# Optimization experiments

Measured on AMD Instinct MI355X. Metric: run time of the kernel, lower is better.

Reference implementation:

```python
import jax, jax.numpy as jnp
import numpy as np

B, S, D = 4, 2048, 1024  # batch, seq_len, input_dimension
KD, VD = 1024, 1024      # key_dim, value_dim


def setup_inputs() -> dict:
    key = jax.random.key(0)
    ks = jax.random.split(key, 9)
    sc_in = 1.0 / np.sqrt(D)
    sc_v = 1.0 / np.sqrt(VD)
    return {
        "x":  jax.random.normal(ks[0], (B, S, D), dtype=jnp.float32),
        "Wq": jax.random.normal(ks[1], (KD, D), dtype=jnp.float32) * sc_in,
        "bq": jax.random.normal(ks[2], (KD,), dtype=jnp.float32) * 0.01,
        "Wk": jax.random.normal(ks[3], (KD, D), dtype=jnp.float32) * sc_in,
        "bk": jax.random.normal(ks[4], (KD,), dtype=jnp.float32) * 0.01,
        "Wv": jax.random.normal(ks[5], (VD, D), dtype=jnp.float32) * sc_in,
        "bv": jax.random.normal(ks[6], (VD,), dtype=jnp.float32) * 0.01,
        "Wo": jax.random.normal(ks[7], (D, VD), dtype=jnp.float32) * sc_v,
        "bo": jax.random.normal(ks[8], (D,), dtype=jnp.float32) * 0.01,
    }


def reference(x, Wq, bq, Wk, bk, Wv, bv, Wo, bo):
    # projections (torch Linear: x @ W.T + b)
    q = jnp.einsum('bsd,kd->bsk', x, Wq) + bq   # (B,S,KD)
    k = jnp.einsum('bsd,kd->bsk', x, Wk) + bk   # (B,S,KD)
    v = jnp.einsum('bsd,vd->bsv', x, Wv) + bv   # (B,S,VD)

    scores = jnp.einsum('bqk,bsk->bqs', q, k) / jnp.sqrt(jnp.float32(KD))  # (B,S,S)

    # sign rescale: scores * sign(scores) (sign(0) mapped to 1) == |scores| with zeros kept
    sign_mask = jnp.sign(scores)
    sign_mask = sign_mask + (sign_mask == 0).astype(jnp.float32)

    # causal mask: lower-triangular (incl diag) multiplied by 1, strict upper -> -inf
    seq = scores.shape[-1]
    causal = jnp.tril(jnp.ones((seq, seq), dtype=bool))
    masked = jnp.where(causal, scores * sign_mask, -jnp.inf)

    weights = jax.nn.softmax(masked, axis=2)            # (B,S,S)
    out = jnp.einsum('bqs,bsv->bqv', weights, v)        # (B,S,VD)
    return jnp.einsum('bqv,dv->bqd', out, Wo) + bo      # (B,S,D)
```

## Files before the change

kernel.cpp:

```cpp
#include <hip/hip_runtime.h>
#include <hip/hip_bf16.h>
#include <cstdint>


#define BM 128

typedef __attribute__((ext_vector_type(8))) __bf16 bf16x8;
typedef __attribute__((ext_vector_type(4))) __bf16 bf16x4;
typedef __attribute__((ext_vector_type(4))) float floatx4;

struct Ptr3 { const float* p[3]; };

__device__ __forceinline__ void async_copy16(const __bf16* g, const __bf16* l) {
  __builtin_amdgcn_global_load_lds(
      (const __attribute__((address_space(1))) unsigned int*)(const void*)g,
      (__attribute__((address_space(3))) unsigned int*)(unsigned)(uintptr_t)(const void*)l,
      16, 0, 0);
}

__device__ __forceinline__ void gemm_core(const __bf16* __restrict__ pA,
                                          const __bf16* __restrict__ pB,
                                          int K, int kBeg, int kEnd, int mb,
                                          int nb, floatx4 (&acc)[4][4]) {
  __shared__ __align__(16) __bf16 As[3][BM * 32];
  __shared__ __align__(16) __bf16 Bs[3][BM * 32];

  const int t = threadIdx.x;
  const int lane = t & 63;
  const int wave = t >> 6;
  const int quad = lane >> 4;
  const int l16 = lane & 15;
  const int wm = wave >> 1;
  const int wn = wave & 1;
  const int qsw = quad ^ ((l16 >> 1) & 3);

  const int srow = t >> 2;
  const int scol = ((t & 3) ^ ((t >> 3) & 3)) * 8;
  const __bf16* gA = pA + (long)(mb * BM + srow) * K + scol;
  const __bf16* gB = pB + (long)(nb * BM + srow) * K + scol;
  const long rowHalf = (long)64 * K;

  auto stage = [&](int kk, int buf) {
    const long ko = (long)kk * 32;
    __bf16* lA = &As[buf][t * 8];
    __bf16* lB = &Bs[buf][t * 8];
    async_copy16(gA + ko, lA);
    async_copy16(gA + ko + rowHalf, lA + 2048);
    async_copy16(gB + ko, lB);
    async_copy16(gB + ko + rowHalf, lB + 2048);
  };

  stage(kBeg, 0);
  stage(kBeg + 1 < kEnd ? kBeg + 1 : kEnd - 1, 1);

  for (int kk = kBeg; kk < kEnd; ++kk) {
    const int cur = (kk - kBeg) % 3;
    asm volatile("s_waitcnt vmcnt(4)" ::: "memory");
    __builtin_amdgcn_s_barrier();
    __builtin_amdgcn_sched_barrier(0);
    {
      const int nxt = kk + 2;
      stage(nxt < kEnd ? nxt : kEnd - 1, (cur + 2) % 3);
    }
    const __bf16* Asp = &As[cur][0];
    const __bf16* Bsp = &Bs[cur][0];
    bf16x8 af[4], bfr[4];
#pragma unroll
    for (int i = 0; i < 4; ++i) {
      af[i] = *(const bf16x8*)&Asp[(wm * 64 + i * 16 + l16) * 32 + qsw * 8];
      bfr[i] = *(const bf16x8*)&Bsp[(wn * 64 + i * 16 + l16) * 32 + qsw * 8];
    }
#pragma unroll
    for (int i = 0; i < 4; ++i)
#pragma unroll
      for (int j = 0; j < 4; ++j)
        acc[i][j] = __builtin_amdgcn_mfma_f32_16x16x32_bf16(af[i], bfr[j],
                                                            acc[i][j], 0, 0, 0);
  }
  __syncthreads();
}

__device__ __forceinline__ void gemm_core256(const __bf16* __restrict__ pA,
                                             const __bf16* __restrict__ pB,
                                             int K, int kBeg, int kEnd, int mb,
                                             int nb, floatx4 (&acc)[8][4]) {
  __shared__ __align__(16) __bf16 As[3][256 * 32];
  __shared__ __align__(16) __bf16 Bs[3][256 * 32];

  const int t = threadIdx.x;
  const int lane = t & 63;
  const int wave = t >> 6;
  const int quad = lane >> 4;
  const int l16 = lane & 15;
  const int wm = wave >> 2;
  const int wn = wave & 3;
  const int qsw = quad ^ ((l16 >> 1) & 3);

  const int srow = t >> 2;
  const int scol = ((t & 3) ^ ((t >> 3) & 3)) * 8;
  const __bf16* gA = pA + (long)(mb * 256 + srow) * K + scol;
  const __bf16* gB = pB + (long)(nb * 256 + srow) * K + scol;
  const long rowHalf = (long)128 * K;

  auto stage = [&](int kk, int buf) {
    const long ko = (long)kk * 32;
    __bf16* lA = &As[buf][t * 8];
    __bf16* lB = &Bs[buf][t * 8];
    async_copy16(gA + ko, lA);
    async_copy16(gA + ko + rowHalf, lA + 4096);
    async_copy16(gB + ko, lB);
    async_copy16(gB + ko + rowHalf, lB + 4096);
  };

  stage(kBeg, 0);
  stage(kBeg + 1 < kEnd ? kBeg + 1 : kEnd - 1, 1);

  for (int kk = kBeg; kk < kEnd; ++kk) {
    const int cur = (kk - kBeg) % 3;
    asm volatile("s_waitcnt vmcnt(4)" ::: "memory");
    __builtin_amdgcn_s_barrier();
    __builtin_amdgcn_sched_barrier(0);
    {
      const int nxt = kk + 2;
      stage(nxt < kEnd ? nxt : kEnd - 1, (cur + 2) % 3);
    }
    const __bf16* Asp = &As[cur][0];
    const __bf16* Bsp = &Bs[cur][0];
    bf16x8 af[8], bfr[4];
#pragma unroll
    for (int j = 0; j < 4; ++j)
      bfr[j] = *(const bf16x8*)&Bsp[(wn * 64 + j * 16 + l16) * 32 + qsw * 8];
#pragma unroll
    for (int i = 0; i < 8; ++i)
      af[i] = *(const bf16x8*)&Asp[(wm * 128 + i * 16 + l16) * 32 + qsw * 8];
#pragma unroll
    for (int i = 0; i < 8; ++i)
#pragma unroll
      for (int j = 0; j < 4; ++j)
        acc[i][j] = __builtin_amdgcn_mfma_f32_16x16x32_bf16(af[i], bfr[j],
                                                            acc[i][j], 0, 0, 0);
  }
  __syncthreads();
}

__global__ void prep2(const float* __restrict__ Wo, Ptr3 tp,
                      const float* __restrict__ bv, const float* __restrict__ bq,
                      const float* __restrict__ bk,
                      __bf16* __restrict__ Wob, __bf16* __restrict__ Wqt,
                      __bf16* __restrict__ Wkt, __bf16* __restrict__ Wvt,
                      float* __restrict__ bvo, float* __restrict__ cscal,
                      float* __restrict__ lsum) {
  __shared__ __bf16 tile[64][66];
  __shared__ float wsum[4];
  const int bid = blockIdx.x;
  const int t = threadIdx.x;
  if (bid < 1024) {
    const long e = ((long)bid * 256 + t) * 4;
    const float4 f = *(const float4*)(Wo + e);
    bf16x4 o;
    o[0] = (__bf16)f.x; o[1] = (__bf16)f.y; o[2] = (__bf16)f.z; o[3] = (__bf16)f.w;
    *(bf16x4*)(Wob + e) = o;
  } else if (bid < 1792) {
    const int seg = (bid - 1024) >> 8;
    const int idx = (bid - 1024) & 255;
    const float* src = tp.p[seg];
    __bf16* dstw = seg == 0 ? Wqt : (seg == 1 ? Wkt : Wvt);
    const int r0 = (idx >> 4) * 64, c0 = (idx & 15) * 64;
#pragma unroll
    for (int e = 0; e < 16; ++e) {
      const int i = e * 256 + t;
      const int r = i >> 6, c = i & 63;
      tile[r][c] = (__bf16)src[(long)(r0 + r) * 1024 + (c0 + c)];
    }
    __syncthreads();
#pragma unroll
    for (int e = 0; e < 16; ++e) {
      const int i = e * 256 + t;
      const int r = i >> 6, c = i & 63;
      dstw[(long)(c0 + r) * 1024 + (r0 + c)] = tile[c][r];
    }
  } else if (bid < 2816) {
    const int d = bid - 1792;
    const float* row = Wo + (long)d * 1024;
    float s = 0.f;
    for (int v = t; v < 1024; v += 256) s += bv[v] * row[v];
#pragma unroll
    for (int off = 32; off > 0; off >>= 1) s += __shfl_down(s, off, 64);
    if ((t & 63) == 0) wsum[t >> 6] = s;
    __syncthreads();
    if (t == 0) bvo[d] = wsum[0] + wsum[1] + wsum[2] + wsum[3];
  } else if (bid == 2816) {
    float s = 0.f;
    for (int i = t; i < 1024; i += 256) s += bq[i] * bk[i];
#pragma unroll
    for (int off = 32; off > 0; off >>= 1) s += __shfl_down(s, off, 64);
    if ((t & 63) == 0) wsum[t >> 6] = s;
    __syncthreads();
    if (t == 0) *cscal = wsum[0] + wsum[1] + wsum[2] + wsum[3];
  } else {
#pragma unroll
    for (int e = 0; e < 8; ++e)
      *(float4*)(lsum + (e * 256 + t) * 4) = float4{0.f, 0.f, 0.f, 0.f};
  }
}

__global__ void __launch_bounds__(256, 3)
gemmA(const __bf16* __restrict__ Wkt, const __bf16* __restrict__ Wqt,
      const __bf16* __restrict__ Wob, const __bf16* __restrict__ Wvt,
      __bf16* __restrict__ Mt, __bf16* __restrict__ Wvo,
      const float* __restrict__ bk, const float* __restrict__ bq,
      float* __restrict__ m1f, float* __restrict__ m2f,
      const float* __restrict__ x, __bf16* __restrict__ xb) {
  const int id = blockIdx.x;
  const int t = threadIdx.x;

  if (id >= 160) {
    const long i = ((long)(id - 160) * 256 + t) * 4;
    const float4 f = *(const float4*)(x + i);
    bf16x4 o;
    o[0] = (__bf16)f.x; o[1] = (__bf16)f.y; o[2] = (__bf16)f.z; o[3] = (__bf16)f.w;
    *(bf16x4*)(xb + i) = o;
    return;
  }
  if (id >= 128) {
    const int q = (id - 128) & 15;
    const bool isM2 = (id - 128) >= 16;
    const __bf16* Wt = isM2 ? Wkt : Wqt;
    const float* bvec = isM2 ? bq : bk;
    float* dst = isM2 ? m2f : m1f;
    const int lane = t & 63, wave = t >> 6, qd = lane >> 4, l16 = lane & 15;
#pragma unroll
    for (int rr = 0; rr < 4; ++rr) {
      const int row = q * 64 + (wave * 4 + qd) * 4 + rr;
      const __bf16* wr = Wt + (long)row * 1024 + l16 * 64;
      const float* bp = bvec + l16 * 64;
      float s = 0.f;
#pragma unroll
      for (int jj = 0; jj < 8; ++jj) {
        bf16x8 wv = *(const bf16x8*)(wr + jj * 8);
#pragma unroll
        for (int e = 0; e < 8; ++e) s += (float)wv[e] * bp[jj * 8 + e];
      }
      s += __shfl_xor(s, 1, 64);
      s += __shfl_xor(s, 2, 64);
      s += __shfl_xor(s, 4, 64);
      s += __shfl_xor(s, 8, 64);
      if (l16 == 0) dst[row] = s;
    }
    return;
  }

  const __bf16 *pA, *pB;
  __bf16* dst;
  int mb, nb;
  if (id < 64) {
    mb = id >> 3; nb = id & 7;
    pA = Wkt; pB = Wqt; dst = Mt;
  } else {
    const int w = id - 64;
    mb = w >> 3; nb = w & 7;
    pA = Wob; pB = Wvt; dst = Wvo;
  }

  floatx4 acc[4][4] = {};
  gemm_core(pA, pB, 1024, 0, 32, mb, nb, acc);

  const int lane = t & 63, wave = t >> 6;
  const int rb = (wave >> 1) * 64 + (lane >> 4) * 4;
  const int cb = (wave & 1) * 64 + (lane & 15);
#pragma unroll
  for (int j4 = 0; j4 < 4; ++j4) {
    const int gc = nb * 128 + cb + j4 * 16;
#pragma unroll
    for (int i = 0; i < 4; ++i) {
      const int gr = mb * BM + rb + i * 16;
#pragma unroll
      for (int r = 0; r < 4; ++r)
        dst[(long)(gr + r) * 1024 + gc] = (__bf16)acc[i][j4][r];
    }
  }
}

__global__ void __launch_bounds__(512, 2)
big1(const __bf16* __restrict__ xb, const __bf16* __restrict__ Mt,
     const __bf16* __restrict__ Wvo, const float* __restrict__ m2f,
     const float* __restrict__ bvo, __bf16* __restrict__ y2,
     __bf16* __restrict__ Ut, const float* __restrict__ m1f,
     const float* __restrict__ cscal, float* __restrict__ uvec,
     int S, int D) {
  const int id = blockIdx.x;
  const int t = threadIdx.x;

  if (id >= 256) {
    const int k = id - 256;
    const int row = k * 64 + (t >> 3);
    const int l8 = t & 7;
    const float c = *cscal;
    const __bf16* xr = xb + (long)row * 1024 + l8 * 128;
    const float* mp = m1f + l8 * 128;
    float s = 0.f;
#pragma unroll
    for (int jj = 0; jj < 16; ++jj) {
      bf16x8 xv = *(const bf16x8*)(xr + jj * 8);
#pragma unroll
      for (int e = 0; e < 8; ++e) s += (float)xv[e] * mp[jj * 8 + e];
    }
    s += __shfl_xor(s, 1, 64);
    s += __shfl_xor(s, 2, 64);
    s += __shfl_xor(s, 4, 64);
    if (l8 == 0) uvec[row] = s + c;
    return;
  }

  const bool isY2 = id < 128;
  const int w = isY2 ? id : id - 128;
  const int mb = w >> 2;
  const int nb = w & 3;
  const __bf16* pB = isY2 ? Mt : Wvo;

  floatx4 acc[8][4] = {};
  gemm_core256(xb, pB, 1024, 0, 32, mb, nb, acc);

  const int lane = t & 63, wave = t >> 6;
  const int quad = lane >> 4, l16 = lane & 15;
  const int wm = wave >> 2, wn = wave & 3;

  if (isY2) {
#pragma unroll
    for (int j = 0; j < 4; ++j) {
      const int gc = nb * 256 + wn * 64 + j * 16 + l16;
      const float bvv = m2f[gc];
#pragma unroll
      for (int i = 0; i < 8; ++i) {
        const int gr = mb * 256 + wm * 128 + i * 16 + quad * 4;
#pragma unroll
        for (int r = 0; r < 4; ++r)
          y2[(long)(gr + r) * 1024 + gc] = (__bf16)(acc[i][j][r] + bvv);
      }
    }
  } else {
    const int bb = (mb * 256) / S;
    const int s0 = mb * 256 - bb * S;
#pragma unroll
    for (int j = 0; j < 4; ++j) {
      const int gc = nb * 256 + wn * 64 + j * 16 + l16;
      const float bv = bvo[gc];
#pragma unroll
      for (int i = 0; i < 8; ++i) {
        const int sr = s0 + wm * 128 + i * 16 + quad * 4;
        bf16x4 o;
#pragma unroll
        for (int r = 0; r < 4; ++r) o[r] = (__bf16)(acc[i][j][r] + bv);
        *(bf16x4*)&Ut[((long)bb * D + gc) * S + sr] = o;
      }
    }
  }
}

__global__ void __launch_bounds__(256, 3)
scoresK(const __bf16* __restrict__ xb, const __bf16* __restrict__ y2,
        const float* __restrict__ uvec, __bf16* __restrict__ P,
        float* __restrict__ lsum, int S, int KD) {
  const int sid = blockIdx.x;
  const int xcd = sid & 7;
  const int r = sid >> 3;
  const int b = r / 17;
  const int ci = r - b * 17;
  const int n1 = xcd + 1;
  const int mb = (ci < n1) ? xcd : (15 - xcd);
  const int nb = (ci < n1) ? ci : (ci - n1);
  const __bf16* pA = y2 + (long)b * S * KD;
  const __bf16* pB = xb + (long)b * S * KD;

  floatx4 acc[4][4] = {};
  gemm_core(pA, pB, KD, 0, KD / 32, mb, nb, acc);

  const int t = threadIdx.x;
  const int lane = t & 63, wave = t >> 6;
  const int l16 = lane & 15;
  const int rb = (wave >> 1) * 64 + (lane >> 4) * 4;
  const int cb = (wave & 1) * 64 + l16;

  __bf16* C = P + (long)b * S * S;
  float* lrow = lsum + (long)b * S;
  const float sc = 0.03125f;
#pragma unroll
  for (int i = 0; i < 4; ++i) {
#pragma unroll
    for (int r4 = 0; r4 < 4; ++r4) {
      const int row = mb * BM + rb + i * 16 + r4;
      const float urow = uvec[(long)b * S + row];
      float psum = 0.f;
#pragma unroll
      for (int j4 = 0; j4 < 4; ++j4) {
        const int col = nb * 128 + cb + j4 * 16;
        const float p =
            (col <= row) ? __expf(fabsf(acc[i][j4][r4] + urow) * sc) : 0.f;
        psum += p;
        C[(long)row * S + col] = (__bf16)p;
      }
      psum += __shfl_xor(psum, 1, 64);
      psum += __shfl_xor(psum, 2, 64);
      psum += __shfl_xor(psum, 4, 64);
      psum += __shfl_xor(psum, 8, 64);
      if (l16 == 0) atomicAdd(&lrow[row], psum);
    }
  }
}

__global__ void __launch_bounds__(256, 3)
gemm_pvo(const __bf16* __restrict__ P, const __bf16* __restrict__ Ut,
         const float* __restrict__ lsum, const float* __restrict__ bo,
         float* __restrict__ out, int S, int D) {
  const int id = blockIdx.x;
  const int xcd = id & 7;
  const int j = id >> 3;
  const int half = j >> 5;
  const int idx = j & 31;
  const int b = idx >> 3;
  const int nb = idx & 7;
  const int mb = half ? xcd : (15 - xcd);

  floatx4 acc[4][4] = {};
  gemm_core(P + (long)b * S * S, Ut + (long)b * D * S, S, 0, 4 * (mb + 1), mb,
            nb, acc);

  const int t = threadIdx.x;
  const int lane = t & 63, wave = t >> 6;
  const int rb = (wave >> 1) * 64 + (lane >> 4) * 4;
  const int cb = (wave & 1) * 64 + (lane & 15);
  const float* lrow = lsum + (long)b * S;

#pragma unroll
  for (int i = 0; i < 4; ++i) {
#pragma unroll
    for (int r = 0; r < 4; ++r) {
      const int row = mb * BM + rb + i * 16 + r;
      const float inv = 1.f / lrow[row];
#pragma unroll
      for (int j4 = 0; j4 < 4; ++j4) {
        const int col = nb * 128 + cb + j4 * 16;
        out[((long)b * S + row) * D + col] = acc[i][j4][r] * inv + bo[col];
      }
    }
  }
}

extern "C" void kernel_launch(void* const* d_in, const int* in_sizes, int n_in,
                              void* d_out, int out_size, void* d_ws, size_t ws_size,
                              hipStream_t stream) {
  const float* x = (const float*)d_in[0];
  const float* Wq = (const float*)d_in[1];
  const float* bq = (const float*)d_in[2];
  const float* Wk = (const float*)d_in[3];
  const float* bk = (const float*)d_in[4];
  const float* Wv = (const float*)d_in[5];
  const float* bv = (const float*)d_in[6];
  const float* Wo = (const float*)d_in[7];
  const float* bo = (const float*)d_in[8];
  float* out = (float*)d_out;

  constexpr int B = 4, S = 2048, D = 1024, KD = 1024;
  constexpr long MB_ = 1024 * 1024;

  char* w = (char*)d_ws;
  __bf16* xb  = (__bf16*)(w);
  __bf16* y2  = (__bf16*)(w + 16 * MB_);
  __bf16* Ut  = (__bf16*)(w + 32 * MB_);
  __bf16* P   = (__bf16*)(w + 48 * MB_);
  __bf16* Wob = (__bf16*)(w + 80 * MB_);
  __bf16* Wqt = (__bf16*)(w + 82 * MB_);
  __bf16* Wkt = (__bf16*)(w + 84 * MB_);
  __bf16* Wvt = (__bf16*)(w + 86 * MB_);
  __bf16* Mt  = (__bf16*)(w + 88 * MB_);
  __bf16* Wvo = (__bf16*)(w + 90 * MB_);
  float* lsum  = (float*)(w + 92 * MB_);
  float* uvec  = (float*)(w + 92 * MB_ + 32768);
  float* bvo   = (float*)(w + 92 * MB_ + 65536);
  float* m2f   = (float*)(w + 92 * MB_ + 69632);
  float* m1f   = (float*)(w + 92 * MB_ + 73728);
  float* cscal = (float*)(w + 92 * MB_ + 77824);

  Ptr3 tp{{Wq, Wk, Wv}};
  prep2<<<2818, 256, 0, stream>>>(Wo, tp, bv, bq, bk, Wob, Wqt, Wkt, Wvt,
                                  bvo, cscal, lsum);

  gemmA<<<8352, 256, 0, stream>>>(Wkt, Wqt, Wob, Wvt, Mt, Wvo, bk, bq,
                                  m1f, m2f, x, xb);

  big1<<<384, 512, 0, stream>>>(xb, Mt, Wvo, m2f, bvo, y2, Ut, m1f, cscal,
                                uvec, S, D);

  scoresK<<<544, 256, 0, stream>>>(xb, y2, uvec, P, lsum, S, KD);

  gemm_pvo<<<512, 256, 0, stream>>>(P, Ut, lsum, bo, out, S, D);
}
```

Baseline: 232.5 us.

## Unify GEMMs on 256x256 8-phase ping-pong pipelined core with 64-wide K tiles

Replaces the 128-tile and 256-tile triple-buffered GEMM cores with one 256x256 core. It uses 64-wide K tiles, double buffering and an 8-phase schedule that interleaves LDS reads, async global loads and MFMA quadrants, with s_setprio raised around the MFMAs. All GEMM kernels (weight products, projections, scores, PV-output) switch to 512-thread blocks with this core. The x-to-bf16 conversion moves into the prep kernel. The intent is more reuse per tile and better overlap of memory with compute. The cost is far fewer blocks (144 and 128) on a 256-CU part, the loss of the XCD-aware scheduling, and causal load imbalance that is now coarser.

```diff
diff --git a/kernel.cpp b/kernel.cpp
--- a/kernel.cpp
+++ b/kernel.cpp
@@ -2,8 +2,6 @@
 #include <hip/hip_bf16.h>
 #include <cstdint>
 
-
-#define BM 128
 
 typedef __attribute__((ext_vector_type(8))) __bf16 bf16x8;
 typedef __attribute__((ext_vector_type(4))) __bf16 bf16x4;
@@ -18,74 +16,12 @@
       16, 0, 0);
 }
 
-__device__ __forceinline__ void gemm_core(const __bf16* __restrict__ pA,
-                                          const __bf16* __restrict__ pB,
-                                          int K, int kBeg, int kEnd, int mb,
-                                          int nb, floatx4 (&acc)[4][4]) {
-  __shared__ __align__(16) __bf16 As[3][BM * 32];
-  __shared__ __align__(16) __bf16 Bs[3][BM * 32];
-
-  const int t = threadIdx.x;
-  const int lane = t & 63;
-  const int wave = t >> 6;
-  const int quad = lane >> 4;
-  const int l16 = lane & 15;
-  const int wm = wave >> 1;
-  const int wn = wave & 1;
-  const int qsw = quad ^ ((l16 >> 1) & 3);
-
-  const int srow = t >> 2;
-  const int scol = ((t & 3) ^ ((t >> 3) & 3)) * 8;
-  const __bf16* gA = pA + (long)(mb * BM + srow) * K + scol;
-  const __bf16* gB = pB + (long)(nb * BM + srow) * K + scol;
-  const long rowHalf = (long)64 * K;
-
-  auto stage = [&](int kk, int buf) {
-    const long ko = (long)kk * 32;
-    __bf16* lA = &As[buf][t * 8];
-    __bf16* lB = &Bs[buf][t * 8];
-    async_copy16(gA + ko, lA);
-    async_copy16(gA + ko + rowHalf, lA + 2048);
-    async_copy16(gB + ko, lB);
-    async_copy16(gB + ko + rowHalf, lB + 2048);
-  };
-
-  stage(kBeg, 0);
-  stage(kBeg + 1 < kEnd ? kBeg + 1 : kEnd - 1, 1);
-
-  for (int kk = kBeg; kk < kEnd; ++kk) {
-    const int cur = (kk - kBeg) % 3;
-    asm volatile("s_waitcnt vmcnt(4)" ::: "memory");
-    __builtin_amdgcn_s_barrier();
-    __builtin_amdgcn_sched_barrier(0);
-    {
-      const int nxt = kk + 2;
-      stage(nxt < kEnd ? nxt : kEnd - 1, (cur + 2) % 3);
-    }
-    const __bf16* Asp = &As[cur][0];
-    const __bf16* Bsp = &Bs[cur][0];
-    bf16x8 af[4], bfr[4];
-#pragma unroll
-    for (int i = 0; i < 4; ++i) {
-      af[i] = *(const bf16x8*)&Asp[(wm * 64 + i * 16 + l16) * 32 + qsw * 8];
-      bfr[i] = *(const bf16x8*)&Bsp[(wn * 64 + i * 16 + l16) * 32 + qsw * 8];
-    }
-#pragma unroll
-    for (int i = 0; i < 4; ++i)
-#pragma unroll
-      for (int j = 0; j < 4; ++j)
-        acc[i][j] = __builtin_amdgcn_mfma_f32_16x16x32_bf16(af[i], bfr[j],
-                                                            acc[i][j], 0, 0, 0);
-  }
-  __syncthreads();
-}
-
-__device__ __forceinline__ void gemm_core256(const __bf16* __restrict__ pA,
-                                             const __bf16* __restrict__ pB,
-                                             int K, int kBeg, int kEnd, int mb,
-                                             int nb, floatx4 (&acc)[8][4]) {
-  __shared__ __align__(16) __bf16 As[3][256 * 32];
-  __shared__ __align__(16) __bf16 Bs[3][256 * 32];
+__device__ __forceinline__ void gemm_core8p(const __bf16* __restrict__ pA,
+                                            const __bf16* __restrict__ pB,
+                                            int K, int nT, int mb, int nb,
+                                            floatx4 (&acc)[8][4]) {
+  __shared__ __align__(16) __bf16 As[2][16384];
+  __shared__ __align__(16) __bf16 Bs[2][16384];
 
   const int t = threadIdx.x;
   const int lane = t & 63;
@@ -94,67 +30,119 @@
   const int l16 = lane & 15;
   const int wm = wave >> 2;
   const int wn = wave & 3;
-  const int qsw = quad ^ ((l16 >> 1) & 3);
-
-  const int srow = t >> 2;
-  const int scol = ((t & 3) ^ ((t >> 3) & 3)) * 8;
-  const __bf16* gA = pA + (long)(mb * 256 + srow) * K + scol;
-  const __bf16* gB = pB + (long)(nb * 256 + srow) * K + scol;
-  const long rowHalf = (long)128 * K;
-
-  auto stage = [&](int kk, int buf) {
-    const long ko = (long)kk * 32;
-    __bf16* lA = &As[buf][t * 8];
-    __bf16* lB = &Bs[buf][t * 8];
-    async_copy16(gA + ko, lA);
-    async_copy16(gA + ko + rowHalf, lA + 4096);
-    async_copy16(gB + ko, lB);
-    async_copy16(gB + ko + rowHalf, lB + 4096);
+
+  const int r0 = t >> 3;
+  const int csw = ((t & 7) ^ (r0 & 7)) * 8;
+  const __bf16* gA = pA + (long)(mb * 256 + r0) * K + csw;
+  const __bf16* gB = pB + (long)(nb * 256 + r0) * K + csw;
+  const long row64 = (long)64 * K;
+  const long row128 = (long)128 * K;
+
+  auto stageA = [&](int kt, int half) {
+    const long ko = (long)kt * 64 + (long)half * row128;
+    __bf16* d = &As[kt & 1][half * 8192 + t * 8];
+    async_copy16(gA + ko, d);
+    async_copy16(gA + ko + row64, d + 4096);
   };
-
-  stage(kBeg, 0);
-  stage(kBeg + 1 < kEnd ? kBeg + 1 : kEnd - 1, 1);
-
-  for (int kk = kBeg; kk < kEnd; ++kk) {
-    const int cur = (kk - kBeg) % 3;
-    asm volatile("s_waitcnt vmcnt(4)" ::: "memory");
-    __builtin_amdgcn_s_barrier();
-    __builtin_amdgcn_sched_barrier(0);
-    {
-      const int nxt = kk + 2;
-      stage(nxt < kEnd ? nxt : kEnd - 1, (cur + 2) % 3);
-    }
-    const __bf16* Asp = &As[cur][0];
-    const __bf16* Bsp = &Bs[cur][0];
-    bf16x8 af[8], bfr[4];
-#pragma unroll
-    for (int j = 0; j < 4; ++j)
-      bfr[j] = *(const bf16x8*)&Bsp[(wn * 64 + j * 16 + l16) * 32 + qsw * 8];
-#pragma unroll
-    for (int i = 0; i < 8; ++i)
-      af[i] = *(const bf16x8*)&Asp[(wm * 128 + i * 16 + l16) * 32 + qsw * 8];
-#pragma unroll
-    for (int i = 0; i < 8; ++i)
-#pragma unroll
-      for (int j = 0; j < 4; ++j)
-        acc[i][j] = __builtin_amdgcn_mfma_f32_16x16x32_bf16(af[i], bfr[j],
-                                                            acc[i][j], 0, 0, 0);
+  auto stageB = [&](int kt, int half) {
+    const long ko = (long)kt * 64 + (long)half * row128;
+    __bf16* d = &Bs[kt & 1][half * 8192 + t * 8];
+    async_copy16(gB + ko, d);
+    async_copy16(gB + ko + row64, d + 4096);
+  };
+  auto cl = [&](int kt) { return kt < nT ? kt : nT - 1; };
+
+  bf16x8 af[4][2], bfr[2][2];
+  auto ldsA = [&](int buf, int ihalf) {
+#pragma unroll
+    for (int i2 = 0; i2 < 4; ++i2) {
+      const int rl = wm * 64 + i2 * 16 + l16;
+      const int rb = ihalf * 8192 + rl * 64;
+      const int key = rl & 7;
+#pragma unroll
+      for (int ks = 0; ks < 2; ++ks)
+        af[i2][ks] = *(const bf16x8*)&As[buf][rb + (((ks * 4 + quad) ^ key) << 3)];
+    }
+  };
+  auto ldsB = [&](int buf, int jhalf) {
+#pragma unroll
+    for (int j2 = 0; j2 < 2; ++j2) {
+      const int rl = wn * 32 + j2 * 16 + l16;
+      const int rb = jhalf * 8192 + rl * 64;
+      const int key = rl & 7;
+#pragma unroll
+      for (int ks = 0; ks < 2; ++ks)
+        bfr[j2][ks] = *(const bf16x8*)&Bs[buf][rb + (((ks * 4 + quad) ^ key) << 3)];
+    }
+  };
+  auto mfmaQ = [&](int ihalf, int jhalf) {
+    __builtin_amdgcn_s_setprio(1);
+#pragma unroll
+    for (int ks = 0; ks < 2; ++ks)
+#pragma unroll
+      for (int i2 = 0; i2 < 4; ++i2)
+#pragma unroll
+        for (int j2 = 0; j2 < 2; ++j2)
+          acc[ihalf * 4 + i2][jhalf * 2 + j2] =
+              __builtin_amdgcn_mfma_f32_16x16x32_bf16(
+                  af[i2][ks], bfr[j2][ks],
+                  acc[ihalf * 4 + i2][jhalf * 2 + j2], 0, 0, 0);
+    __builtin_amdgcn_s_setprio(0);
+  };
+
+#define VM6 asm volatile("s_waitcnt vmcnt(6)" ::: "memory")
+#define PHASE(LDSOP, STAGEOP, WAITOP, IH, JH)                 \
+  LDSOP;                                                      \
+  STAGEOP;                                                    \
+  WAITOP;                                                     \
+  __builtin_amdgcn_sched_barrier(0);                          \
+  __builtin_amdgcn_s_barrier();                               \
+  asm volatile("s_waitcnt lgkmcnt(0)" ::: "memory");          \
+  __builtin_amdgcn_sched_barrier(0);                          \
+  mfmaQ(IH, JH);                                              \
+  __builtin_amdgcn_s_barrier();
+
+  stageA(0, 0); stageB(0, 0); stageB(0, 1); stageA(0, 1);
+  stageA(1, 0); stageB(1, 1); stageA(1, 1);
+  VM6;
+  __builtin_amdgcn_s_barrier();
+  __builtin_amdgcn_sched_barrier(0);
+
+  const int nIter = nT >> 1;
+  for (int it = 0, T = 0; it < nIter; ++it, T += 2) {
+    PHASE((ldsA(0, 0), ldsB(0, 0)), stageB(cl(T + 1), 0), (void)0, 0, 0)
+    PHASE(ldsB(0, 1),               stageA(cl(T + 2), 0), (void)0, 0, 1)
+    PHASE(ldsA(0, 1),               stageB(cl(T + 2), 1), (void)0, 1, 1)
+    PHASE(ldsB(0, 0),               stageA(cl(T + 2), 1), VM6,     1, 0)
+    PHASE((ldsA(1, 0), ldsB(1, 0)), stageB(cl(T + 2), 0), (void)0, 0, 0)
+    PHASE(ldsB(1, 1),               stageA(cl(T + 3), 0), (void)0, 0, 1)
+    PHASE(ldsA(1, 1),               stageB(cl(T + 3), 1), (void)0, 1, 1)
+    PHASE(ldsB(1, 0),               stageA(cl(T + 3), 1), VM6,     1, 0)
   }
   __syncthreads();
-}
-
-__global__ void prep2(const float* __restrict__ Wo, Ptr3 tp,
-                      const float* __restrict__ bv, const float* __restrict__ bq,
-                      const float* __restrict__ bk,
-                      __bf16* __restrict__ Wob, __bf16* __restrict__ Wqt,
-                      __bf16* __restrict__ Wkt, __bf16* __restrict__ Wvt,
-                      float* __restrict__ bvo, float* __restrict__ cscal,
-                      float* __restrict__ lsum) {
+#undef PHASE
+#undef VM6
+}
+
+
+__global__ void prep2b(const float* __restrict__ Wo, Ptr3 tp,
+                       const float* __restrict__ bv, const float* __restrict__ bq,
+                       const float* __restrict__ bk, const float* __restrict__ x,
+                       __bf16* __restrict__ Wob, __bf16* __restrict__ Wqt,
+                       __bf16* __restrict__ Wkt, __bf16* __restrict__ Wvt,
+                       __bf16* __restrict__ xb, float* __restrict__ bvo,
+                       float* __restrict__ cscal, float* __restrict__ lsum) {
   __shared__ __bf16 tile[64][66];
   __shared__ float wsum[4];
   const int bid = blockIdx.x;
   const int t = threadIdx.x;
-  if (bid < 1024) {
+  if (bid >= 2818) {
+    const long i = ((long)(bid - 2818) * 256 + t) * 4;
+    const float4 f = *(const float4*)(x + i);
+    bf16x4 o;
+    o[0] = (__bf16)f.x; o[1] = (__bf16)f.y; o[2] = (__bf16)f.z; o[3] = (__bf16)f.w;
+    *(bf16x4*)(xb + i) = o;
+  } else if (bid < 1024) {
     const long e = ((long)bid * 256 + t) * 4;
     const float4 f = *(const float4*)(Wo + e);
     bf16x4 o;
@@ -204,79 +192,62 @@
   }
 }
 
-__global__ void __launch_bounds__(256, 3)
-gemmA(const __bf16* __restrict__ Wkt, const __bf16* __restrict__ Wqt,
+__global__ void __launch_bounds__(512, 2)
+gemmW(const __bf16* __restrict__ Wkt, const __bf16* __restrict__ Wqt,
       const __bf16* __restrict__ Wob, const __bf16* __restrict__ Wvt,
       __bf16* __restrict__ Mt, __bf16* __restrict__ Wvo,
       const float* __restrict__ bk, const float* __restrict__ bq,
-      float* __restrict__ m1f, float* __restrict__ m2f,
-      const float* __restrict__ x, __bf16* __restrict__ xb) {
+      float* __restrict__ m1f, float* __restrict__ m2f) {
   const int id = blockIdx.x;
   const int t = threadIdx.x;
 
-  if (id >= 160) {
-    const long i = ((long)(id - 160) * 256 + t) * 4;
-    const float4 f = *(const float4*)(x + i);
-    bf16x4 o;
-    o[0] = (__bf16)f.x; o[1] = (__bf16)f.y; o[2] = (__bf16)f.z; o[3] = (__bf16)f.w;
-    *(bf16x4*)(xb + i) = o;
-    return;
-  }
-  if (id >= 128) {
-    const int q = (id - 128) & 15;
-    const bool isM2 = (id - 128) >= 16;
+  if (id >= 32) {
+    const int g = id - 32;
+    const bool isM2 = g >= 16;
+    const int q = g & 15;
     const __bf16* Wt = isM2 ? Wkt : Wqt;
     const float* bvec = isM2 ? bq : bk;
     float* dst = isM2 ? m2f : m1f;
-    const int lane = t & 63, wave = t >> 6, qd = lane >> 4, l16 = lane & 15;
-#pragma unroll
-    for (int rr = 0; rr < 4; ++rr) {
-      const int row = q * 64 + (wave * 4 + qd) * 4 + rr;
-      const __bf16* wr = Wt + (long)row * 1024 + l16 * 64;
-      const float* bp = bvec + l16 * 64;
-      float s = 0.f;
-#pragma unroll
-      for (int jj = 0; jj < 8; ++jj) {
-        bf16x8 wv = *(const bf16x8*)(wr + jj * 8);
-#pragma unroll
-        for (int e = 0; e < 8; ++e) s += (float)wv[e] * bp[jj * 8 + e];
-      }
-      s += __shfl_xor(s, 1, 64);
-      s += __shfl_xor(s, 2, 64);
-      s += __shfl_xor(s, 4, 64);
-      s += __shfl_xor(s, 8, 64);
-      if (l16 == 0) dst[row] = s;
-    }
+    const int row = q * 64 + (t >> 3);
+    const int l8 = t & 7;
+    const __bf16* wr = Wt + (long)row * 1024 + l8 * 128;
+    const float* bp = bvec + l8 * 128;
+    float s = 0.f;
+#pragma unroll
+    for (int jj = 0; jj < 16; ++jj) {
+      bf16x8 wv = *(const bf16x8*)(wr + jj * 8);
+#pragma unroll
+      for (int e = 0; e < 8; ++e) s += (float)wv[e] * bp[jj * 8 + e];
+    }
+    s += __shfl_xor(s, 1, 64);
+    s += __shfl_xor(s, 2, 64);
+    s += __shfl_xor(s, 4, 64);
+    if (l8 == 0) dst[row] = s;
     return;
   }
 
-  const __bf16 *pA, *pB;
-  __bf16* dst;
-  int mb, nb;
-  if (id < 64) {
-    mb = id >> 3; nb = id & 7;
-    pA = Wkt; pB = Wqt; dst = Mt;
-  } else {
-    const int w = id - 64;
-    mb = w >> 3; nb = w & 7;
-    pA = Wob; pB = Wvt; dst = Wvo;
-  }
-
-  floatx4 acc[4][4] = {};
-  gemm_core(pA, pB, 1024, 0, 32, mb, nb, acc);
+  const bool isMt = id < 16;
+  const int w = isMt ? id : id - 16;
+  const int mb = w >> 2, nb = w & 3;
+  const __bf16* pA = isMt ? Wkt : Wob;
+  const __bf16* pB = isMt ? Wqt : Wvt;
+  __bf16* dst = isMt ? Mt : Wvo;
+
+  floatx4 acc[8][4] = {};
+  gemm_core8p(pA, pB, 1024, 16, mb, nb, acc);
 
   const int lane = t & 63, wave = t >> 6;
-  const int rb = (wave >> 1) * 64 + (lane >> 4) * 4;
-  const int cb = (wave & 1) * 64 + (lane & 15);
-#pragma unroll
-  for (int j4 = 0; j4 < 4; ++j4) {
-    const int gc = nb * 128 + cb + j4 * 16;
-#pragma unroll
-    for (int i = 0; i < 4; ++i) {
-      const int gr = mb * BM + rb + i * 16;
+  const int quad = lane >> 4, l16 = lane & 15;
+  const int wm = wave >> 2, wn = wave & 3;
+#pragma unroll
+  for (int j = 0; j < 4; ++j) {
+    const int gc = nb * 256 + (j >> 1) * 128 + wn * 32 + (j & 1) * 16 + l16;
+#pragma unroll
+    for (int i = 0; i < 8; ++i) {
+      const int gr = mb * 256 + (i >> 2) * 128 + wm * 64 + (i & 3) * 16 + quad * 4;
 #pragma unroll
       for (int r = 0; r < 4; ++r)
-        dst[(long)(gr + r) * 1024 + gc] = (__bf16)acc[i][j4][r];
+        dst[(long)(gr + r) * 1024 + gc] = (__bf16)acc[i][j][r];
     }
   }
 }
@@ -319,7 +290,7 @@
   const __bf16* pB = isY2 ? Mt : Wvo;
 
   floatx4 acc[8][4] = {};
-  gemm_core256(xb, pB, 1024, 0, 32, mb, nb, acc);
+  gemm_core8p(xb, pB, 1024, 16, mb, nb, acc);
 
   const int lane = t & 63, wave = t >> 6;
   const int quad = lane >> 4, l16 = lane & 15;
@@ -328,11 +299,11 @@
   if (isY2) {
 #pragma unroll
     for (int j = 0; j < 4; ++j) {
-      const int gc = nb * 256 + wn * 64 + j * 16 + l16;
+      const int gc = nb * 256 + (j >> 1) * 128 + wn * 32 + (j & 1) * 16 + l16;
       const float bvv = m2f[gc];
 #pragma unroll
       for (int i = 0; i < 8; ++i) {
-        const int gr = mb * 256 + wm * 128 + i * 16 + quad * 4;
+        const int gr = mb * 256 + (i >> 2) * 128 + wm * 64 + (i & 3) * 16 + quad * 4;
 #pragma unroll
         for (int r = 0; r < 4; ++r)
           y2[(long)(gr + r) * 1024 + gc] = (__bf16)(acc[i][j][r] + bvv);
@@ -343,11 +314,11 @@
     const int s0 = mb * 256 - bb * S;
 #pragma unroll
     for (int j = 0; j < 4; ++j) {
-      const int gc = nb * 256 + wn * 64 + j * 16 + l16;
+      const int gc = nb * 256 + (j >> 1) * 128 + wn * 32 + (j & 1) * 16 + l16;
       const float bv = bvo[gc];
 #pragma unroll
       for (int i = 0; i < 8; ++i) {
-        const int sr = s0 + wm * 128 + i * 16 + quad * 4;
+        const int sr = s0 + (i >> 2) * 128 + wm * 64 + (i & 3) * 16 + quad * 4;
         bf16x4 o;
 #pragma unroll
         for (int r = 0; r < 4; ++r) o[r] = (__bf16)(acc[i][j][r] + bv);
@@ -357,45 +328,40 @@
   }
 }
 
-__global__ void __launch_bounds__(256, 3)
-scoresK(const __bf16* __restrict__ xb, const __bf16* __restrict__ y2,
+__global__ void __launch_bounds__(512, 2)
+scoresP(const __bf16* __restrict__ xb, const __bf16* __restrict__ y2,
         const float* __restrict__ uvec, __bf16* __restrict__ P,
         float* __restrict__ lsum, int S, int KD) {
-  const int sid = blockIdx.x;
-  const int xcd = sid & 7;
-  const int r = sid >> 3;
-  const int b = r / 17;
-  const int ci = r - b * 17;
-  const int n1 = xcd + 1;
-  const int mb = (ci < n1) ? xcd : (15 - xcd);
-  const int nb = (ci < n1) ? ci : (ci - n1);
-  const __bf16* pA = y2 + (long)b * S * KD;
-  const __bf16* pB = xb + (long)b * S * KD;
-
-  floatx4 acc[4][4] = {};
-  gemm_core(pA, pB, KD, 0, KD / 32, mb, nb, acc);
+  const int id = blockIdx.x;
+  const int b = id / 36;
+  const int r = id - b * 36;
+  int mb = 0;
+  while ((mb + 1) * (mb + 2) / 2 <= r) ++mb;
+  const int nb = r - mb * (mb + 1) / 2;
+
+  floatx4 acc[8][4] = {};
+  gemm_core8p(y2 + (long)b * S * KD, xb + (long)b * S * KD, KD, 16, mb, nb, acc);
 
   const int t = threadIdx.x;
   const int lane = t & 63, wave = t >> 6;
-  const int l16 = lane & 15;
-  const int rb = (wave >> 1) * 64 + (lane >> 4) * 4;
-  const int cb = (wave & 1) * 64 + l16;
+  const int quad = lane >> 4, l16 = lane & 15;
+  const int wm = wave >> 2, wn = wave & 3;
 
   __bf16* C = P + (long)b * S * S;
   float* lrow = lsum + (long)b * S;
   const float sc = 0.03125f;
 #pragma unroll
-  for (int i = 0; i < 4; ++i) {
+  for (int i = 0; i < 8; ++i) {
 #pragma unroll
     for (int r4 = 0; r4 < 4; ++r4) {
-      const int row = mb * BM + rb + i * 16 + r4;
+      const int row = mb * 256 + (i >> 2) * 128 + wm * 64 + (i & 3) * 16 + quad * 4 + r4;
       const float urow = uvec[(long)b * S + row];
       float psum = 0.f;
 #pragma unroll
-      for (int j4 = 0; j4 < 4; ++j4) {
-        const int col = nb * 128 + cb + j4 * 16;
+      for (int j = 0; j < 4; ++j) {
+        const int col = nb * 256 + (j >> 1) * 128 + wn * 32 + (j & 1) * 16 + l16;
         const float p =
-            (col <= row) ? __expf(fabsf(acc[i][j4][r4] + urow) * sc) : 0.f;
+            (col <= row) ? __expf(fabsf(acc[i][j][r4] + urow) * sc) : 0.f;
         psum += p;
         C[(long)row * S + col] = (__bf16)p;
       }
@@ -408,39 +374,36 @@
   }
 }
 
-__global__ void __launch_bounds__(256, 3)
+__global__ void __launch_bounds__(512, 2)
 gemm_pvo(const __bf16* __restrict__ P, const __bf16* __restrict__ Ut,
          const float* __restrict__ lsum, const float* __restrict__ bo,
          float* __restrict__ out, int S, int D) {
   const int id = blockIdx.x;
-  const int xcd = id & 7;
-  const int j = id >> 3;
-  const int half = j >> 5;
-  const int idx = j & 31;
-  const int b = idx >> 3;
-  const int nb = idx & 7;
-  const int mb = half ? xcd : (15 - xcd);
-
-  floatx4 acc[4][4] = {};
-  gemm_core(P + (long)b * S * S, Ut + (long)b * D * S, S, 0, 4 * (mb + 1), mb,
-            nb, acc);
+  const int b = id >> 5;
+  const int idx = id & 31;
+  const int mb = idx >> 2;
+  const int nb = idx & 3;
+
+  floatx4 acc[8][4] = {};
+  gemm_core8p(P + (long)b * S * S, Ut + (long)b * D * S, S, 4 * (mb + 1), mb,
+              nb, acc);
 
   const int t = threadIdx.x;
   const int lane = t & 63, wave = t >> 6;
-  const int rb = (wave >> 1) * 64 + (lane >> 4) * 4;
-  const int cb = (wave & 1) * 64 + (lane & 15);
+  const int quad = lane >> 4, l16 = lane & 15;
+  const int wm = wave >> 2, wn = wave & 3;
   const float* lrow = lsum + (long)b * S;
 
 #pragma unroll
-  for (int i = 0; i < 4; ++i) {
+  for (int i = 0; i < 8; ++i) {
 #pragma unroll
     for (int r = 0; r < 4; ++r) {
-      const int row = mb * BM + rb + i * 16 + r;
+      const int row = mb * 256 + (i >> 2) * 128 + wm * 64 + (i & 3) * 16 + quad * 4 + r;
       const float inv = 1.f / lrow[row];
 #pragma unroll
-      for (int j4 = 0; j4 < 4; ++j4) {
-        const int col = nb * 128 + cb + j4 * 16;
-        out[((long)b * S + row) * D + col] = acc[i][j4][r] * inv + bo[col];
+      for (int j = 0; j < 4; ++j) {
+        const int col = nb * 256 + (j >> 1) * 128 + wn * 32 + (j & 1) * 16 + l16;
+        out[((long)b * S + row) * D + col] = acc[i][j][r] * inv + bo[col];
       }
     }
   }
@@ -482,16 +445,15 @@
   float* cscal = (float*)(w + 92 * MB_ + 77824);
 
   Ptr3 tp{{Wq, Wk, Wv}};
-  prep2<<<2818, 256, 0, stream>>>(Wo, tp, bv, bq, bk, Wob, Wqt, Wkt, Wvt,
-                                  bvo, cscal, lsum);
-
-  gemmA<<<8352, 256, 0, stream>>>(Wkt, Wqt, Wob, Wvt, Mt, Wvo, bk, bq,
-                                  m1f, m2f, x, xb);
+  prep2b<<<11010, 256, 0, stream>>>(Wo, tp, bv, bq, bk, x, Wob, Wqt, Wkt,
+                                    Wvt, xb, bvo, cscal, lsum);
+
+  gemmW<<<64, 512, 0, stream>>>(Wkt, Wqt, Wob, Wvt, Mt, Wvo, bk, bq, m1f, m2f);
 
   big1<<<384, 512, 0, stream>>>(xb, Mt, Wvo, m2f, bvo, y2, Ut, m1f, cscal,
                                 uvec, S, D);
 
-  scoresK<<<544, 256, 0, stream>>>(xb, y2, uvec, P, lsum, S, KD);
-
-  gemm_pvo<<<512, 256, 0, stream>>>(P, Ut, lsum, bo, out, S, D);
-}
+  scoresP<<<144, 512, 0, stream>>>(xb, y2, uvec, P, lsum, S, KD);
+
+  gemm_pvo<<<128, 512, 0, stream>>>(P, Ut, lsum, bo, out, S, D);
+}
```

After: 269.1 us. +15.7%, slower.
